# Kernel tuning notes

Measured on AMD Instinct MI355X. Metric: run time of the kernel, lower is better.

Reference implementation:

```python
import jax, jax.numpy as jnp
import numpy as np


def setup_inputs() -> dict:
    key = jax.random.key(0)
    k1, k2 = jax.random.split(key)
    x = jax.random.normal(k1, (32, 3, 512, 512), dtype=jnp.float32)
    p = jax.random.uniform(k2, (32, 4), dtype=jnp.float32)
    return {"x": x, "p": p}


def _reflect(coord, size):
    # PyTorch grid_sample reflection padding, align_corners=False:
    # reflect about borders at -0.5 and size-0.5 (span = size), then clip.
    span = float(size)
    c = jnp.abs(coord + 0.5)
    flips = jnp.floor(c / span)
    extra = c - flips * span
    c = jnp.where(jnp.mod(flips, 2.0) == 0.0, extra, span - extra) - 0.5
    return jnp.clip(c, 0.0, size - 1.0)


def _bilinear_sample(img, ix, iy, W, H):
    # img: [C,H,W]; ix,iy: [H,W] pixel-space coords already reflected into [0,size-1]
    ix0f = jnp.floor(ix)
    iy0f = jnp.floor(iy)
    fx = ix - ix0f
    fy = iy - iy0f
    x0 = jnp.clip(ix0f.astype(jnp.int32), 0, W - 1)
    x1 = jnp.clip(ix0f.astype(jnp.int32) + 1, 0, W - 1)
    y0 = jnp.clip(iy0f.astype(jnp.int32), 0, H - 1)
    y1 = jnp.clip(iy0f.astype(jnp.int32) + 1, 0, H - 1)
    v00 = img[:, y0, x0]  # [C,H,W]
    v01 = img[:, y0, x1]
    v10 = img[:, y1, x0]
    v11 = img[:, y1, x1]
    return (v00 * (1.0 - fx) * (1.0 - fy)
            + v01 * fx * (1.0 - fy)
            + v10 * (1.0 - fx) * fy
            + v11 * fx * fy)


def reference(x, p):
    B, C, H, W = x.shape
    tx, ty, th, ts = p[:, 0], p[:, 1], p[:, 2], p[:, 3]
    c, s = jnp.cos(th), jnp.sin(th)
    # affine_grid base coords, align_corners=False: centers of pixels in [-1,1]
    xs = (jnp.arange(W, dtype=x.dtype) + 0.5) * (2.0 / W) - 1.0  # [W]
    ys = (jnp.arange(H, dtype=x.dtype) + 0.5) * (2.0 / H) - 1.0  # [H]
    a = (ts * c)[:, None, None]
    b = (-ts * s)[:, None, None]
    d = (ts * s)[:, None, None]
    e = (ts * c)[:, None, None]
    gx = a * xs[None, None, :] + b * ys[None, :, None] + tx[:, None, None]  # [B,H,W]
    gy = d * xs[None, None, :] + e * ys[None, :, None] + ty[:, None, None]  # [B,H,W]
    # unnormalize to pixel space (align_corners=False)
    ix = ((gx + 1.0) * W - 1.0) * 0.5
    iy = ((gy + 1.0) * H - 1.0) * 0.5
    ix = _reflect(ix, W)
    iy = _reflect(iy, H)
    out = jax.vmap(lambda img, jx, jy: _bilinear_sample(img, jx, jy, W, H))(x, ix, iy)
    return out
```

## Files before the change

### kernel.cpp

```cpp
#include <hip/hip_runtime.h>


#define B_ 32
#define C_ 3
#define H_ 512
#define W_ 512
#define TILE 32
#define BOX 56
#define LSTRIDE 60
#define CH_WORDS (BOX * LSTRIDE)

typedef float f32x4 __attribute__((ext_vector_type(4)));

__device__ __forceinline__ float reflect512(float coord) {
    const float c = fabsf(coord + 0.5f);
    const float m = c - floorf(c * (1.0f / 1024.0f)) * 1024.0f;
    const float t = 512.0f - fabsf(m - 512.0f);
    return fminf(fmaxf(t - 0.5f, 0.0f), 511.0f);
}

__global__ __launch_bounds__(256, 4)
void st_kernel(const float* __restrict__ x, const float* __restrict__ p,
               float* __restrict__ out) {
    __shared__ float smem[C_ * CH_WORDS + LSTRIDE];

    const int tid = threadIdx.x;
    const int b   = blockIdx.z;

    const float tx = p[b * 4 + 0];
    const float ty = p[b * 4 + 1];
    const float th = p[b * 4 + 2];
    const float ts = p[b * 4 + 3];
    const float cth = __cosf(th), sth = __sinf(th);
    const float a  =  ts * cth;
    const float bb = -ts * sth;
    const float d  =  ts * sth;

    const float xs_c = ((float)(blockIdx.x * TILE) + 16.0f) * (2.0f / W_) - 1.0f;
    const float ys_c = ((float)(blockIdx.y * TILE) + 16.0f) * (2.0f / H_) - 1.0f;
    const float gxc = a * xs_c + bb * ys_c + tx;
    const float gyc = d * xs_c + a  * ys_c + ty;
    const float rcx = reflect512(((gxc + 1.0f) * W_ - 1.0f) * 0.5f);
    const float rcy = reflect512(((gyc + 1.0f) * H_ - 1.0f) * 0.5f);
    const float ext = 16.0f * (fabsf(a) + fabsf(bb)) + 3.0f;
    int bx0 = (int)floorf(rcx - ext);
    bx0 = (min(max(bx0, 0), W_ - BOX)) & ~3;
    int by0 = (int)floorf(rcy - ext);
    by0 = min(max(by0, 0), H_ - BOX);

    const size_t plane = (size_t)H_ * W_;
    const float* img = x + (size_t)b * C_ * plane;

    {
        const int c4 = tid & 15;
        const int r0 = tid >> 4;
        if (c4 < 15) {
            #pragma unroll
            for (int ch = 0; ch < C_; ++ch) {
                #pragma unroll
                for (int rg = 0; rg < 4; ++rg) {
                    const int r = r0 + rg * 16;
                    if (r < BOX) {
                        f32x4 v = (f32x4)(0.0f);
                        if (c4 < 14)
                            v = *reinterpret_cast<const f32x4*>(
                                img + ch * plane + (size_t)(by0 + r) * W_ + (bx0 + c4 * 4));
                        *reinterpret_cast<f32x4*>(
                            &smem[ch * CH_WORDS + r * LSTRIDE + c4 * 4]) = v;
                    }
                }
            }
        }
        if (tid < 15)
            *reinterpret_cast<f32x4*>(&smem[C_ * CH_WORDS + tid * 4]) = (f32x4)(0.0f);
    }
    __syncthreads();

    const int lr   = tid >> 3;
    const int lc   = (tid & 7) * 4;
    const int row  = blockIdx.y * TILE + lr;
    const int col0 = blockIdx.x * TILE + lc;

    const float ysn = ((float)row  + 0.5f) * (2.0f / H_) - 1.0f;
    const float xsn = ((float)col0 + 0.5f) * (2.0f / W_) - 1.0f;
    float ix = ((a * xsn + bb * ysn + tx + 1.0f) * W_ - 1.0f) * 0.5f;
    float iy = ((d * xsn + a  * ysn + ty + 1.0f) * H_ - 1.0f) * 0.5f;

    const int koff = by0 * LSTRIDE + bx0;
    float acc[C_][4];

    #pragma unroll
    for (int k = 0; k < 4; ++k) {
        const float rx  = reflect512(ix);
        const float ry  = reflect512(iy);
        const float x0f = floorf(rx);
        const float y0f = floorf(ry);
        const float fx  = rx - x0f;
        const float fy  = ry - y0f;
        const float ox  = 1.0f - fx;
        const float oy  = 1.0f - fy;
        const float w00 = ox * oy, w01 = fx * oy, w10 = ox * fy, w11 = fx * fy;

        const int idx = (int)y0f * LSTRIDE + (int)x0f - koff;
        const float* s = &smem[idx];
        #pragma unroll
        for (int ch = 0; ch < C_; ++ch) {
            const float* sc = s + ch * CH_WORDS;
            acc[ch][k] = sc[0] * w00 + sc[1] * w01
                       + sc[LSTRIDE] * w10 + sc[LSTRIDE + 1] * w11;
        }
        ix += a;
        iy += d;
    }

    float* o = out + (size_t)b * C_ * plane + (size_t)row * W_ + col0;
    #pragma unroll
    for (int ch = 0; ch < C_; ++ch) {
        const f32x4 v = {acc[ch][0], acc[ch][1], acc[ch][2], acc[ch][3]};
        __builtin_nontemporal_store(v, reinterpret_cast<f32x4*>(o + (size_t)ch * plane));
    }
}

extern "C" void kernel_launch(void* const* d_in, const int* in_sizes, int n_in,
                              void* d_out, int out_size, void* d_ws, size_t ws_size,
                              hipStream_t stream) {
    const float* x = (const float*)d_in[0];
    const float* p = (const float*)d_in[1];
    float* out = (float*)d_out;

    dim3 block(256, 1, 1);
    dim3 grid(W_ / TILE, H_ / TILE, B_);
    st_kernel<<<grid, block, 0, stream>>>(x, p, out);
}
```

Before: 208.5 us.

## Split blocks per channel, size staging box to footprint, and swizzle block order

Each block now handles one channel of a 32x32 tile, with a flat grid that is remapped so consecutive hardware blocks are spread across XCDs. The shared-memory staging box is sized to the actual transformed footprint (variable rows and columns) instead of a fixed 56x56, which cuts redundant global loads when the scale is small. Shared memory per block shrinks, allowing eight blocks per CU. The trade-off is three times as many blocks, each recomputing the transform parameters, plus more divergent load loops. The footprint clamp to 57 rows and 15 vector columns could also produce out-of-box reads for large scales.

```diff
diff --git a/kernel.cpp b/kernel.cpp
--- a/kernel.cpp
+++ b/kernel.cpp
@@ -6,9 +6,8 @@
 #define H_ 512
 #define W_ 512
 #define TILE 32
-#define BOX 56
 #define LSTRIDE 60
-#define CH_WORDS (BOX * LSTRIDE)
+#define SMEM_WORDS (57 * LSTRIDE + 64)
 
 typedef float f32x4 __attribute__((ext_vector_type(4)));
 
@@ -19,13 +18,21 @@
     return fminf(fmaxf(t - 0.5f, 0.0f), 511.0f);
 }
 
-__global__ __launch_bounds__(256, 4)
+__global__ __launch_bounds__(256, 8)
 void st_kernel(const float* __restrict__ x, const float* __restrict__ p,
                float* __restrict__ out) {
-    __shared__ float smem[C_ * CH_WORDS + LSTRIDE];
+    __shared__ float smem[SMEM_WORDS];
 
     const int tid = threadIdx.x;
-    const int b   = blockIdx.z;
+
+    const int bid = blockIdx.x;
+    const int wid = (bid & 7) * 3072 + (bid >> 3);
+    const int ch  = wid >> 13;
+    const int rst = wid & 8191;
+    const int b   = rst >> 8;
+    const int til = rst & 255;
+    const int tlx = til & 15;
+    const int tly = til >> 4;
 
     const float tx = p[b * 4 + 0];
     const float ty = p[b * 4 + 1];
@@ -36,50 +43,47 @@
     const float bb = -ts * sth;
     const float d  =  ts * sth;
 
-    const float xs_c = ((float)(blockIdx.x * TILE) + 16.0f) * (2.0f / W_) - 1.0f;
-    const float ys_c = ((float)(blockIdx.y * TILE) + 16.0f) * (2.0f / H_) - 1.0f;
+    const float xs_c = ((float)(tlx * TILE) + 16.0f) * (2.0f / W_) - 1.0f;
+    const float ys_c = ((float)(tly * TILE) + 16.0f) * (2.0f / H_) - 1.0f;
     const float gxc = a * xs_c + bb * ys_c + tx;
     const float gyc = d * xs_c + a  * ys_c + ty;
     const float rcx = reflect512(((gxc + 1.0f) * W_ - 1.0f) * 0.5f);
     const float rcy = reflect512(((gyc + 1.0f) * H_ - 1.0f) * 0.5f);
     const float ext = 16.0f * (fabsf(a) + fabsf(bb)) + 3.0f;
-    int bx0 = (int)floorf(rcx - ext);
-    bx0 = (min(max(bx0, 0), W_ - BOX)) & ~3;
-    int by0 = (int)floorf(rcy - ext);
-    by0 = min(max(by0, 0), H_ - BOX);
+
+    int bx0 = max((int)floorf(rcx - ext), 0) & ~3;
+    const int xhi = min((int)ceilf(rcx + ext) + 1, W_);
+    int nw4 = (xhi - bx0 + 3) >> 2;
+    nw4 = min(min(nw4, 15), (W_ - bx0) >> 2);
+
+    int by0 = max((int)floorf(rcy - ext), 0);
+    const int yhi = min((int)ceilf(rcy + ext) + 1, H_);
+    const int nrows = min(yhi - by0, 57);
 
     const size_t plane = (size_t)H_ * W_;
-    const float* img = x + (size_t)b * C_ * plane;
+    const float* img = x + ((size_t)b * C_ + ch) * plane;
 
     {
         const int c4 = tid & 15;
-        const int r0 = tid >> 4;
-        if (c4 < 15) {
-            #pragma unroll
-            for (int ch = 0; ch < C_; ++ch) {
-                #pragma unroll
-                for (int rg = 0; rg < 4; ++rg) {
-                    const int r = r0 + rg * 16;
-                    if (r < BOX) {
-                        f32x4 v = (f32x4)(0.0f);
-                        if (c4 < 14)
-                            v = *reinterpret_cast<const f32x4*>(
-                                img + ch * plane + (size_t)(by0 + r) * W_ + (bx0 + c4 * 4));
-                        *reinterpret_cast<f32x4*>(
-                            &smem[ch * CH_WORDS + r * LSTRIDE + c4 * 4]) = v;
-                    }
-                }
+        const float* gp = img + (size_t)by0 * W_ + bx0;
+        for (int r = tid >> 4; r < nrows; r += 16) {
+            float* ld = &smem[r * LSTRIDE];
+            if (c4 < nw4) {
+                const f32x4 v = *reinterpret_cast<const f32x4*>(gp + (size_t)r * W_ + c4 * 4);
+                *reinterpret_cast<f32x4*>(ld + c4 * 4) = v;
+            } else if (c4 == nw4 && nw4 < 15) {
+                *reinterpret_cast<f32x4*>(ld + c4 * 4) = (f32x4)(0.0f);
             }
         }
-        if (tid < 15)
-            *reinterpret_cast<f32x4*>(&smem[C_ * CH_WORDS + tid * 4]) = (f32x4)(0.0f);
+        if (tid < 16)
+            *reinterpret_cast<f32x4*>(&smem[nrows * LSTRIDE + tid * 4]) = (f32x4)(0.0f);
     }
     __syncthreads();
 
     const int lr   = tid >> 3;
     const int lc   = (tid & 7) * 4;
-    const int row  = blockIdx.y * TILE + lr;
-    const int col0 = blockIdx.x * TILE + lc;
+    const int row  = tly * TILE + lr;
+    const int col0 = tlx * TILE + lc;
 
     const float ysn = ((float)row  + 0.5f) * (2.0f / H_) - 1.0f;
     const float xsn = ((float)col0 + 0.5f) * (2.0f / W_) - 1.0f;
@@ -87,7 +91,7 @@
     float iy = ((d * xsn + a  * ysn + ty + 1.0f) * H_ - 1.0f) * 0.5f;
 
     const int koff = by0 * LSTRIDE + bx0;
-    float acc[C_][4];
+    float acc[4];
 
     #pragma unroll
     for (int k = 0; k < 4; ++k) {
@@ -103,22 +107,15 @@
 
         const int idx = (int)y0f * LSTRIDE + (int)x0f - koff;
         const float* s = &smem[idx];
-        #pragma unroll
-        for (int ch = 0; ch < C_; ++ch) {
-            const float* sc = s + ch * CH_WORDS;
-            acc[ch][k] = sc[0] * w00 + sc[1] * w01
-                       + sc[LSTRIDE] * w10 + sc[LSTRIDE + 1] * w11;
-        }
+        acc[k] = s[0] * w00 + s[1] * w01
+               + s[LSTRIDE] * w10 + s[LSTRIDE + 1] * w11;
         ix += a;
         iy += d;
     }
 
-    float* o = out + (size_t)b * C_ * plane + (size_t)row * W_ + col0;
-    #pragma unroll
-    for (int ch = 0; ch < C_; ++ch) {
-        const f32x4 v = {acc[ch][0], acc[ch][1], acc[ch][2], acc[ch][3]};
-        __builtin_nontemporal_store(v, reinterpret_cast<f32x4*>(o + (size_t)ch * plane));
-    }
+    float* o = out + ((size_t)b * C_ + ch) * plane + (size_t)row * W_ + col0;
+    const f32x4 v = {acc[0], acc[1], acc[2], acc[3]};
+    __builtin_nontemporal_store(v, reinterpret_cast<f32x4*>(o));
 }
 
 extern "C" void kernel_launch(void* const* d_in, const int* in_sizes, int n_in,
@@ -129,6 +126,6 @@
     float* out = (float*)d_out;
 
     dim3 block(256, 1, 1);
-    dim3 grid(W_ / TILE, H_ / TILE, B_);
+    dim3 grid((W_ / TILE) * (H_ / TILE) * B_ * C_, 1, 1);
     st_kernel<<<grid, block, 0, stream>>>(x, p, out);
 }
```

After: 186.1 us. 10.8% less time.
